# Optimization experiments

Measured on AMD Instinct MI355X. Metric: run time of the kernel, lower is better.

## Reference

```python
import jax, jax.numpy as jnp
import numpy as np

N = 50000   # nodes
E = 800000  # edges (avg degree 16)
D = 128     # feature dim
H = 4       # heads
Dh = D // H # per-head dim = 32


def setup_inputs() -> dict:
    key = jax.random.key(0)
    ks = jax.random.split(key, 12)
    inp = {
        "x": jax.random.normal(ks[0], (N, D), jnp.float32),
        "edge_index": jax.random.randint(ks[1], (2, E), 0, N, dtype=jnp.int64),
    }
    i = 2
    for l in range(2):
        for nm in ("q", "k", "v", "s"):
            inp[f"{nm}_w{l}"] = jax.random.normal(ks[i], (D, D), jnp.float32) / np.float32(np.sqrt(D))
            inp[f"{nm}_b{l}"] = jnp.zeros((D,), jnp.float32)
        i += 1
    return inp


def _transformer_conv(x, src, dst, qw, qb, kw, kb, vw, vb, sw, sb):
    """PyG TransformerConv: concat heads, root_weight skip, softmax over in-edges."""
    n = x.shape[0]
    q = (x @ qw + qb).reshape(n, H, Dh)
    k = (x @ kw + kb).reshape(n, H, Dh)
    v = (x @ vw + vb).reshape(n, H, Dh)
    # per-edge attention logits [E, H]
    logits = jnp.einsum('ehd,ehd->eh', q[dst], k[src]) / jnp.sqrt(jnp.float32(Dh))
    # segment softmax over edges grouped by destination node
    m = jax.ops.segment_max(logits, dst, num_segments=n)          # [N, H]
    e = jnp.exp(logits - m[dst])                                  # [E, H]
    s = jax.ops.segment_sum(e, dst, num_segments=n)               # [N, H]
    alpha = e / (s[dst] + 1e-16)                                  # [E, H]
    msg = v[src] * alpha[:, :, None]                              # [E, H, Dh]
    out = jax.ops.segment_sum(msg, dst, num_segments=n)           # [N, H, Dh]
    out = out.reshape(n, H * Dh)
    return out + x @ sw + sb  # root skip (lin_skip)


def reference(x, edge_index,
              q_w0, q_b0, k_w0, k_b0, v_w0, v_b0, s_w0, s_b0,
              q_w1, q_b1, k_w1, k_b1, v_w1, v_b1, s_w1, s_b1):
    src, dst = edge_index[0], edge_index[1]
    h = _transformer_conv(x, src, dst, q_w0, q_b0, k_w0, k_b0, v_w0, v_b0, s_w0, s_b0)
    h = jax.nn.relu(h)  # dropout is identity in eval mode
    h = _transformer_conv(h, src, dst, q_w1, q_b1, k_w1, k_b1, v_w1, v_b1, s_w1, s_b1)
    return h
```

## Files before the change

kernel.cpp:

```cpp
#include <hip/hip_runtime.h>
#include <math.h>

#define NN 50000
#define NR 50016
#define EE 800000
#define SCALE 0.17677669529663687f
#define MAXDEG 64
#define NRANGE 4
#define RSPAN (NN / NRANGE)
#define NSLICE 250
#define ESLICE (EE / NSLICE)

typedef __attribute__((ext_vector_type(8))) short short8;
typedef __attribute__((ext_vector_type(4))) float floatx4;
typedef __attribute__((ext_vector_type(4))) int intx4;
typedef unsigned short ushort_t;

#if defined(__has_builtin)
#  if __has_builtin(__builtin_amdgcn_fdot2_f32_bf16)
#    define HAVE_BF16_DOT2 1
#  endif
#endif
#ifndef HAVE_BF16_DOT2
#  define HAVE_BF16_DOT2 0
#endif
#if HAVE_BF16_DOT2
typedef __attribute__((ext_vector_type(2))) __bf16 bf16x2;
#endif

static __device__ __forceinline__ float bf2f(ushort_t u) {
    union { unsigned int i; float f; } x; x.i = ((unsigned int)u) << 16; return x.f;
}
static __device__ __forceinline__ ushort_t f2bf(float f) {
    union { float fv; unsigned int i; } x; x.fv = f;
    unsigned int lsb = (x.i >> 16) & 1u;
    x.i += 0x7fffu + lsb;
    return (ushort_t)(x.i >> 16);
}

static __device__ __forceinline__ float dot8bf(short8 k8, short8 q8, float p) {
#if HAVE_BF16_DOT2
    union { short8 s; unsigned int u[4]; } ku, qu;
    ku.s = k8; qu.s = q8;
#pragma unroll
    for (int i = 0; i < 4; ++i) {
        union { unsigned int u; bf16x2 h; } a, b;
        a.u = ku.u[i]; b.u = qu.u[i];
        p = __builtin_amdgcn_fdot2_f32_bf16(a.h, b.h, p, false);
    }
#else
#pragma unroll
    for (int i = 0; i < 8; ++i)
        p += bf2f((ushort_t)k8[i]) * bf2f((ushort_t)q8[i]);
#endif
    return p;
}

__global__ void k_detect(const int* __restrict__ ei, int* __restrict__ flag) {
    int any = 0;
#pragma unroll
    for (int i = 0; i < 4; ++i) any |= ei[2 * (threadIdx.x * 4 + i) + 1];
    unsigned long long b = __ballot(any != 0);
    if (threadIdx.x == 0) *flag = (b == 0ull) ? 1 : 0;
}

static __device__ __forceinline__ int edge_src(const int* ei, int is64, int e) {
    return is64 ? ei[2 * e] : ei[e];
}
static __device__ __forceinline__ int edge_dst(const int* ei, int is64, int e) {
    return is64 ? ei[2 * (EE + e)] : ei[EE + e];
}

__global__ void k_prep_weights(const float* q0, const float* k0,
                               const float* v0, const float* s0,
                               const float* q1, const float* k1,
                               const float* v1, const float* s1,
                               ushort_t* wt0, ushort_t* wt1) {
    int widx = blockIdx.x >> 3;
    const float* src =
        (widx == 0) ? q0 : (widx == 1) ? k0 : (widx == 2) ? v0 : (widx == 3) ? s0 :
        (widx == 4) ? q1 : (widx == 5) ? k1 : (widx == 6) ? v1 : s1;
    ushort_t* dst = ((widx < 4) ? wt0 : wt1) + (size_t)(widx & 3) * (128 * 128);
    int it0 = (blockIdx.x & 7) * 8;
    for (int it = it0; it < it0 + 8; ++it) {
        int idx = it * 256 + threadIdx.x;
        int j    = idx & 7;
        int lane = (idx >> 3) & 63;
        int t    = (idx >> 9) & 7;
        int kkb  = idx >> 12;
        int kk = kkb * 32 + (lane >> 4) * 8 + j;
        int c  = t * 16 + (lane & 15);
        dst[idx] = f2bf(src[kk * 128 + c]);
    }
}

__global__ void k_compact(const int* __restrict__ ei, const int* __restrict__ flag,
                          int* __restrict__ pairs) {
    int e = blockIdx.x * blockDim.x + threadIdx.x;
    if (e < EE) {
        int is64 = *flag;
        pairs[2 * e]     = edge_dst(ei, is64, e);
        pairs[2 * e + 1] = edge_src(ei, is64, e);
    }
}

__global__ __launch_bounds__(256) void k_fillp(
    const int* __restrict__ pairs,
    int* __restrict__ cnt, int* __restrict__ col) {
    int range = blockIdx.x & (NRANGE - 1);
    int slice = blockIdx.x >> 2;
    int lo = range * RSPAN, hi = lo + RSPAN;
    const int* p = pairs + (size_t)slice * ESLICE * 2;
    for (int i = threadIdx.x; i < ESLICE / 2; i += 256) {
        intx4 v = *(const intx4*)(p + i * 4);
        int d0 = v[0], d1 = v[2];
        if (d0 >= lo && d0 < hi) {
            int pos = atomicAdd(&cnt[d0], 1);
            if (pos < MAXDEG) col[d0 * MAXDEG + pos] = v[1];
        }
        if (d1 >= lo && d1 < hi) {
            int pos = atomicAdd(&cnt[d1], 1);
            if (pos < MAXDEG) col[d1 * MAXDEG + pos] = v[3];
        }
    }
}

template <bool F32A>
__global__ __launch_bounds__(256) void k_gemm_qkvs(
    const void* __restrict__ Av,
    const ushort_t* __restrict__ Wp,
    const float* __restrict__ qb, const float* __restrict__ kb,
    const float* __restrict__ vb, const float* __restrict__ sb,
    ushort_t* __restrict__ Q, ushort_t* __restrict__ KV,
    ushort_t* __restrict__ S) {
    __shared__ ushort_t sA[32][136];
    int wave = threadIdx.x >> 6;
    int lane = threadIdx.x & 63;
    int quad = lane >> 4;
    int lm = lane & 15;
    int row0 = blockIdx.x * 32;

    if (F32A) {
        int r  = threadIdx.x >> 3;
        int c0 = (threadIdx.x & 7) * 16;
        int rr = row0 + r; if (rr > NN - 1) rr = NN - 1;
        const float* srcp = (const float*)Av + (size_t)rr * 128 + c0;
        floatx4 v0 = *(const floatx4*)(srcp);
        floatx4 v1 = *(const floatx4*)(srcp + 4);
        floatx4 v2 = *(const floatx4*)(srcp + 8);
        floatx4 v3 = *(const floatx4*)(srcp + 12);
        short8 o0, o1;
#pragma unroll
        for (int i = 0; i < 4; ++i) {
            o0[i]     = (short)f2bf(v0[i]); o0[i + 4] = (short)f2bf(v1[i]);
            o1[i]     = (short)f2bf(v2[i]); o1[i + 4] = (short)f2bf(v3[i]);
        }
        *(short8*)&sA[r][c0]     = o0;
        *(short8*)&sA[r][c0 + 8] = o1;
    } else {
        const ushort_t* A = (const ushort_t*)Av;
#pragma unroll
        for (int it = 0; it < 2; ++it) {
            int r = it * 16 + (threadIdx.x >> 4);
            int c = (threadIdx.x & 15) * 8;
            *(short8*)&sA[r][c] = *(const short8*)(A + (size_t)(row0 + r) * 128 + c);
        }
    }
    __syncthreads();

    const ushort_t* wp = Wp + (size_t)wave * 16384;
    floatx4 acc[2][8];
#pragma unroll
    for (int rt = 0; rt < 2; ++rt)
#pragma unroll
        for (int t = 0; t < 8; ++t) acc[rt][t] = (floatx4)0.0f;

#pragma unroll
    for (int kkb = 0; kkb < 4; ++kkb) {
        short8 a0 = *(const short8*)&sA[lm][kkb * 32 + quad * 8];
        short8 a1 = *(const short8*)&sA[16 + lm][kkb * 32 + quad * 8];
#pragma unroll
        for (int t = 0; t < 8; ++t) {
            short8 b = *(const short8*)(wp + (size_t)((kkb * 8 + t) * 64 + lane) * 8);
            acc[0][t] = __builtin_amdgcn_mfma_f32_16x16x32_bf16(a0, b, acc[0][t], 0, 0, 0);
            acc[1][t] = __builtin_amdgcn_mfma_f32_16x16x32_bf16(a1, b, acc[1][t], 0, 0, 0);
        }
    }

    const float* bias = (wave == 0) ? qb : (wave == 1) ? kb : (wave == 2) ? vb : sb;
    ushort_t* O     = (wave == 0) ? Q  : (wave == 3) ? S : KV;
    int       strd  = (wave == 1 || wave == 2) ? 256 : 128;
    int       cofs  = (wave == 2) ? 128 : 0;
#pragma unroll
    for (int rt = 0; rt < 2; ++rt)
#pragma unroll
        for (int t = 0; t < 8; ++t) {
            int c = t * 16 + lm;
            float bv = bias[c];
#pragma unroll
            for (int r = 0; r < 4; ++r) {
                int row = row0 + rt * 16 + quad * 4 + r;
                O[(size_t)row * strd + cofs + c] = f2bf(acc[rt][t][r] + bv);
            }
        }
}

__global__ __launch_bounds__(256) void k_attn(
    const ushort_t* __restrict__ Q, const ushort_t* __restrict__ KV,
    const ushort_t* __restrict__ S,
    const int* __restrict__ cnt, const int* __restrict__ col,
    ushort_t* __restrict__ outb, float* __restrict__ outf, int do_relu) {
    int grp = threadIdx.x >> 3;
    int sub = threadIdx.x & 7;
    int node = blockIdx.x * 32 + grp;
    if (node >= NN) return;

    const ushort_t* qrow = Q + (size_t)node * 128 + sub * 16;
    short8 qa  = *(const short8*)qrow;
    short8 qb8 = *(const short8*)(qrow + 8);
    const ushort_t* srow = S + (size_t)node * 128 + sub * 16;
    short8 sa  = *(const short8*)srow;
    short8 sb8 = *(const short8*)(srow + 8);

    int deg = cnt[node]; if (deg > MAXDEG) deg = MAXDEG;
    const int* crow = col + node * MAXDEG;

    float l = 0.f;
    float acc[16];
#pragma unroll
    for (int i = 0; i < 16; ++i) acc[i] = 0.f;

    if (deg > 0) {
        int s = crow[0];
        const ushort_t* kv = KV + (size_t)s * 256 + sub * 16;
        short8 ka  = *(const short8*)kv;
        short8 kb8 = *(const short8*)(kv + 8);
        short8 va  = *(const short8*)(kv + 128);
        short8 vb8 = *(const short8*)(kv + 136);
#pragma unroll 2
        for (int e = 0; e < deg; ++e) {
            int en = (e + 1 < deg) ? (e + 1) : e;
            int s2 = crow[en];
            const ushort_t* kv2 = KV + (size_t)s2 * 256 + sub * 16;
            short8 nka  = *(const short8*)kv2;
            short8 nkb  = *(const short8*)(kv2 + 8);
            short8 nva  = *(const short8*)(kv2 + 128);
            short8 nvb  = *(const short8*)(kv2 + 136);

            float p = 0.f;
            p = dot8bf(ka, qa, p);
            p = dot8bf(kb8, qb8, p);
            p += __shfl_xor(p, 1);
            float w = __expf(p * SCALE);
            l += w;
#pragma unroll
            for (int i = 0; i < 8; ++i) {
                acc[i]     += w * bf2f((ushort_t)va[i]);
                acc[i + 8] += w * bf2f((ushort_t)vb8[i]);
            }
            ka = nka; kb8 = nkb; va = nva; vb8 = nvb;
        }
    }

    float inv = 1.0f / (l + 1e-16f);
    float o[16];
#pragma unroll
    for (int i = 0; i < 8; ++i) {
        o[i]     = acc[i]     * inv + bf2f((ushort_t)sa[i]);
        o[i + 8] = acc[i + 8] * inv + bf2f((ushort_t)sb8[i]);
    }
    if (do_relu)
#pragma unroll
        for (int i = 0; i < 16; ++i) o[i] = fmaxf(o[i], 0.f);
    if (outb) {
        short8 ob0, ob1;
#pragma unroll
        for (int i = 0; i < 8; ++i) {
            ob0[i] = (short)f2bf(o[i]);
            ob1[i] = (short)f2bf(o[i + 8]);
        }
        *(short8*)(outb + (size_t)node * 128 + sub * 16)     = ob0;
        *(short8*)(outb + (size_t)node * 128 + sub * 16 + 8) = ob1;
    }
    if (outf) {
#pragma unroll
        for (int t = 0; t < 4; ++t) {
            floatx4 ov;
#pragma unroll
            for (int i = 0; i < 4; ++i) ov[i] = o[t * 4 + i];
            *(floatx4*)(outf + (size_t)node * 128 + sub * 16 + t * 4) = ov;
        }
    }
}

extern "C" void kernel_launch(void* const* d_in, const int* in_sizes, int n_in,
                              void* d_out, int out_size, void* d_ws, size_t ws_size,
                              hipStream_t stream) {
    const float* x  = (const float*)d_in[0];
    const int*   ei = (const int*)d_in[1];
    const float* qw0 = (const float*)d_in[2];
    const float* qb0 = (const float*)d_in[3];
    const float* kw0 = (const float*)d_in[4];
    const float* kb0 = (const float*)d_in[5];
    const float* vw0 = (const float*)d_in[6];
    const float* vb0 = (const float*)d_in[7];
    const float* sw0 = (const float*)d_in[8];
    const float* sb0 = (const float*)d_in[9];
    const float* qw1 = (const float*)d_in[10];
    const float* qb1 = (const float*)d_in[11];
    const float* kw1 = (const float*)d_in[12];
    const float* kb1 = (const float*)d_in[13];
    const float* vw1 = (const float*)d_in[14];
    const float* vb1 = (const float*)d_in[15];
    const float* sw1 = (const float*)d_in[16];
    const float* sb1 = (const float*)d_in[17];

    char* ws = (char*)d_ws;
    size_t off = 0;
    auto alloc = [&](size_t bytes) -> void* {
        void* p = ws + off;
        off = (off + bytes + 255) & ~(size_t)255;
        return p;
    };
    int* flag       = (int*)alloc(4);
    int* cnt        = (int*)alloc((size_t)NN * 4);
    int* pairs      = (int*)alloc((size_t)EE * 8);
    int* colp       = (int*)alloc((size_t)NN * MAXDEG * 4);
    ushort_t* wt0   = (ushort_t*)alloc((size_t)512 * 128 * 2);
    ushort_t* wt1   = (ushort_t*)alloc((size_t)512 * 128 * 2);
    ushort_t* Q     = (ushort_t*)alloc((size_t)NR * 128 * 2);
    ushort_t* KV    = (ushort_t*)alloc((size_t)NR * 256 * 2);
    ushort_t* S     = (ushort_t*)alloc((size_t)NR * 128 * 2);
    ushort_t* h1b   = (ushort_t*)alloc((size_t)NR * 128 * 2);
    (void)ws_size; (void)in_sizes; (void)n_in; (void)out_size;

    (void)hipMemsetAsync(cnt, 0, (size_t)NN * 4, stream);
    k_detect<<<1, 64, 0, stream>>>(ei, flag);
    k_prep_weights<<<64, 256, 0, stream>>>(qw0, kw0, vw0, sw0, qw1, kw1, vw1, sw1, wt0, wt1);
    k_compact<<<(EE + 255) / 256, 256, 0, stream>>>(ei, flag, pairs);
    k_fillp<<<NSLICE * NRANGE, 256, 0, stream>>>(pairs, cnt, colp);

    k_gemm_qkvs<true><<<NR / 32, 256, 0, stream>>>(x, wt0, qb0, kb0, vb0, sb0, Q, KV, S);
    k_attn<<<(NN + 31) / 32, 256, 0, stream>>>(Q, KV, S, cnt, colp, h1b, nullptr, 1);

    k_gemm_qkvs<false><<<NR / 32, 256, 0, stream>>>(h1b, wt1, qb1, kb1, vb1, sb1, Q, KV, S);
    k_attn<<<(NN + 31) / 32, 256, 0, stream>>>(Q, KV, S, cnt, colp, nullptr,
                                               (float*)d_out, 0);
}
```

Measured before the change: 335.9 us.

## Batch attention edge gathers eight at a time with 64-thread blocks

```diff
diff --git a/kernel.cpp b/kernel.cpp
--- a/kernel.cpp
+++ b/kernel.cpp
@@ -205,64 +205,76 @@
         }
 }
 
-__global__ __launch_bounds__(256) void k_attn(
+__global__ __launch_bounds__(64, 4) void k_attn(
     const ushort_t* __restrict__ Q, const ushort_t* __restrict__ KV,
     const ushort_t* __restrict__ S,
     const int* __restrict__ cnt, const int* __restrict__ col,
     ushort_t* __restrict__ outb, float* __restrict__ outf, int do_relu) {
     int grp = threadIdx.x >> 3;
     int sub = threadIdx.x & 7;
-    int node = blockIdx.x * 32 + grp;
-    if (node >= NN) return;
+    int node = blockIdx.x * 8 + grp;
 
     const ushort_t* qrow = Q + (size_t)node * 128 + sub * 16;
     short8 qa  = *(const short8*)qrow;
     short8 qb8 = *(const short8*)(qrow + 8);
+
+    int deg = cnt[node]; if (deg > MAXDEG) deg = MAXDEG;
+    const int* crow = col + node * MAXDEG;
+
+    float l = 0.f;
+    float acc[16];
+#pragma unroll
+    for (int i = 0; i < 16; ++i) acc[i] = 0.f;
+
+    for (int c0 = 0; c0 < deg; c0 += 8) {
+        int nval = deg - c0;
+        intx4 i0 = *(const intx4*)(crow + c0);
+        intx4 i1 = *(const intx4*)(crow + c0 + 4);
+        int sidx[8];
+#pragma unroll
+        for (int i = 0; i < 4; ++i) {
+            sidx[i]     = (i < nval)     ? i0[i] : 0;
+            sidx[i + 4] = (i + 4 < nval) ? i1[i] : 0;
+        }
+        short8 ka[8], kb8[8];
+#pragma unroll
+        for (int i = 0; i < 8; ++i) {
+            const ushort_t* kvp = KV + (size_t)sidx[i] * 256 + sub * 16;
+            ka[i]  = *(const short8*)kvp;
+            kb8[i] = *(const short8*)(kvp + 8);
+        }
+        float w[8];
+#pragma unroll
+        for (int i = 0; i < 8; ++i) {
+            float p = 0.f;
+            p = dot8bf(ka[i], qa, p);
+            p = dot8bf(kb8[i], qb8, p);
+            p += __shfl_xor(p, 1);
+            float wv = __expf(p * SCALE);
+            w[i] = (i < nval) ? wv : 0.f;
+            l += w[i];
+        }
+        short8 va[8], vb8[8];
+#pragma unroll
+        for (int i = 0; i < 8; ++i) {
+            const ushort_t* kvp = KV + (size_t)sidx[i] * 256 + sub * 16;
+            va[i]  = *(const short8*)(kvp + 128);
+            vb8[i] = *(const short8*)(kvp + 136);
+        }
+#pragma unroll
+        for (int i = 0; i < 8; ++i) {
+#pragma unroll
+            for (int j = 0; j < 8; ++j) {
+                acc[j]     += w[i] * bf2f((ushort_t)va[i][j]);
+                acc[j + 8] += w[i] * bf2f((ushort_t)vb8[i][j]);
+            }
+        }
+    }
+
+    float inv = 1.0f / (l + 1e-16f);
     const ushort_t* srow = S + (size_t)node * 128 + sub * 16;
     short8 sa  = *(const short8*)srow;
     short8 sb8 = *(const short8*)(srow + 8);
-
-    int deg = cnt[node]; if (deg > MAXDEG) deg = MAXDEG;
-    const int* crow = col + node * MAXDEG;
-
-    float l = 0.f;
-    float acc[16];
-#pragma unroll
-    for (int i = 0; i < 16; ++i) acc[i] = 0.f;
-
-    if (deg > 0) {
-        int s = crow[0];
-        const ushort_t* kv = KV + (size_t)s * 256 + sub * 16;
-        short8 ka  = *(const short8*)kv;
-        short8 kb8 = *(const short8*)(kv + 8);
-        short8 va  = *(const short8*)(kv + 128);
-        short8 vb8 = *(const short8*)(kv + 136);
-#pragma unroll 2
-        for (int e = 0; e < deg; ++e) {
-            int en = (e + 1 < deg) ? (e + 1) : e;
-            int s2 = crow[en];
-            const ushort_t* kv2 = KV + (size_t)s2 * 256 + sub * 16;
-            short8 nka  = *(const short8*)kv2;
-            short8 nkb  = *(const short8*)(kv2 + 8);
-            short8 nva  = *(const short8*)(kv2 + 128);
-            short8 nvb  = *(const short8*)(kv2 + 136);
-
-            float p = 0.f;
-            p = dot8bf(ka, qa, p);
-            p = dot8bf(kb8, qb8, p);
-            p += __shfl_xor(p, 1);
-            float w = __expf(p * SCALE);
-            l += w;
-#pragma unroll
-            for (int i = 0; i < 8; ++i) {
-                acc[i]     += w * bf2f((ushort_t)va[i]);
-                acc[i + 8] += w * bf2f((ushort_t)vb8[i]);
-            }
-            ka = nka; kb8 = nkb; va = nva; vb8 = nvb;
-        }
-    }
-
-    float inv = 1.0f / (l + 1e-16f);
     float o[16];
 #pragma unroll
     for (int i = 0; i < 8; ++i) {
@@ -341,9 +353,9 @@
     k_fillp<<<NSLICE * NRANGE, 256, 0, stream>>>(pairs, cnt, colp);
 
     k_gemm_qkvs<true><<<NR / 32, 256, 0, stream>>>(x, wt0, qb0, kb0, vb0, sb0, Q, KV, S);
-    k_attn<<<(NN + 31) / 32, 256, 0, stream>>>(Q, KV, S, cnt, colp, h1b, nullptr, 1);
+    k_attn<<<NN / 8, 64, 0, stream>>>(Q, KV, S, cnt, colp, h1b, nullptr, 1);
 
     k_gemm_qkvs<false><<<NR / 32, 256, 0, stream>>>(h1b, wt1, qb1, kb1, vb1, sb1, Q, KV, S);
-    k_attn<<<(NN + 31) / 32, 256, 0, stream>>>(Q, KV, S, cnt, colp, nullptr,
-                                               (float*)d_out, 0);
-}
+    k_attn<<<NN / 8, 64, 0, stream>>>(Q, KV, S, cnt, colp, nullptr,
+                                      (float*)d_out, 0);
+}
```

After: 401.9 us. +19.6%, slower.
